# Kernel optimization log

Hardware: AMD Instinct MI355X
Metric: run time of the kernel (lower is better)

Reference implementation:

```python
import jax, jax.numpy as jnp
import numpy as np

K, N = 4096, 4096
GROUP_SIZE = 128
N_GROUPS = N // GROUP_SIZE  # 32
BATCH, SEQ = 4, 2048
NBITS = 4


def setup_inputs() -> dict:
    key = jax.random.key(0)
    ks = jax.random.split(key, 7)
    x = jax.random.normal(ks[0], (BATCH, SEQ, N), dtype=jnp.float32)
    W_q = jax.random.randint(ks[1], (K, N), 0, 2 ** NBITS, dtype=jnp.int32)
    scales = jax.random.uniform(ks[2], (K, N_GROUPS, 1), dtype=jnp.float32) * 0.05 + 0.001
    zeros = jax.random.uniform(ks[3], (K, N_GROUPS, 1), dtype=jnp.float32) * (2 ** NBITS)
    mu1 = jax.random.uniform(ks[4], (N,), dtype=jnp.float32) + 0.5  # per-column sinkhorn factor
    mu2 = jax.random.uniform(ks[5], (K,), dtype=jnp.float32) + 0.5  # per-row sinkhorn factor
    bias = jax.random.normal(ks[6], (K,), dtype=jnp.float32)
    return {"x": x, "W_q": W_q, "scales": scales, "zeros": zeros,
            "mu1": mu1, "mu2": mu2, "bias": bias}


def reference(x, W_q, scales, zeros, mu1, mu2, bias):
    input_dtype = x.dtype
    n_groups = scales.shape[1]
    group_size = W_q.shape[1] // n_groups
    # group-wise dequant: [K, n_groups, group_size]
    Q_g = W_q.astype(jnp.float32).reshape(K, n_groups, group_size)
    W_deq_norm = (Q_g - zeros) * scales
    # undo sinkhorn row/col normalization
    W_deq = W_deq_norm.reshape(K, N) * mu2[:, None] * mu1[None, :]
    W_deq = W_deq.astype(input_dtype)
    # linear: x [B,S,N] @ W_deq.T [N,K] + bias [K]
    return jnp.einsum('bsn,kn->bsk', x, W_deq) + bias
```

## Files before the change

kernel.cpp:

```cpp
#include <hip/hip_runtime.h>
#include <hip/hip_bf16.h>
#include <stdint.h>

#define M_DIM 8192
#define N_C   4096
#define K_OUT 4096
#define NGRP  32
#define NT    (N_C / 32)

typedef __attribute__((ext_vector_type(8))) short bf16x8;
typedef __attribute__((ext_vector_type(4))) float f32x4;

__device__ __forceinline__ unsigned short f2b(float f) {
  unsigned u = __float_as_uint(f);
  return (unsigned short)((u + 0x7fffu + ((u >> 16) & 1u)) >> 16);
}

__device__ __forceinline__ void gload_lds16(const void* g, void* l) {
  __builtin_amdgcn_global_load_lds(
      (const __attribute__((address_space(1))) void*)g,
      (__attribute__((address_space(3))) void*)l,
      16, 0, 0);
}

__global__ void convert_x_kernel(const float* __restrict__ x,
                                 unsigned short* __restrict__ xb) {
  const int total = (M_DIM * N_C) / 8;
  const int stride = gridDim.x * blockDim.x;
  for (int i = blockIdx.x * blockDim.x + threadIdx.x; i < total; i += stride) {
    const float4* p = (const float4*)(x + (size_t)i * 8);
    float4 a = p[0];
    float4 b = p[1];
    union { unsigned short u[8]; uint4 v; } o;
    o.u[0] = f2b(a.x); o.u[1] = f2b(a.y); o.u[2] = f2b(a.z); o.u[3] = f2b(a.w);
    o.u[4] = f2b(b.x); o.u[5] = f2b(b.y); o.u[6] = f2b(b.z); o.u[7] = f2b(b.w);
    *(uint4*)(xb + (size_t)i * 8) = o.v;
  }
}

__global__ void dequant_w_kernel(const int* __restrict__ Wq,
                                 const float* __restrict__ scales,
                                 const float* __restrict__ zeros,
                                 const float* __restrict__ mu1,
                                 const float* __restrict__ mu2,
                                 unsigned short* __restrict__ wb) {
  const int total = (K_OUT * N_C) / 8;
  const int stride = gridDim.x * blockDim.x;
  for (int i = blockIdx.x * blockDim.x + threadIdx.x; i < total; i += stride) {
    const int k  = i >> 9;
    const int nc = (i & 511) << 3;
    const int g  = nc >> 7;
    const float s = scales[k * NGRP + g];
    const float z = zeros[k * NGRP + g];
    const float f  = s * mu2[k];
    const float zf = z * f;
    const int4* q4 = (const int4*)(Wq + (size_t)k * N_C + nc);
    int4 q0 = q4[0], q1 = q4[1];
    const float4* m4 = (const float4*)(mu1 + nc);
    float4 m0 = m4[0], m1 = m4[1];
    union { unsigned short u[8]; uint4 v; } o;
    o.u[0] = f2b(((float)q0.x * f - zf) * m0.x);
    o.u[1] = f2b(((float)q0.y * f - zf) * m0.y);
    o.u[2] = f2b(((float)q0.z * f - zf) * m0.z);
    o.u[3] = f2b(((float)q0.w * f - zf) * m0.w);
    o.u[4] = f2b(((float)q1.x * f - zf) * m1.x);
    o.u[5] = f2b(((float)q1.y * f - zf) * m1.y);
    o.u[6] = f2b(((float)q1.z * f - zf) * m1.z);
    o.u[7] = f2b(((float)q1.w * f - zf) * m1.w);
    *(uint4*)(wb + (size_t)i * 8) = o.v;
  }
}

__global__ __launch_bounds__(512) void gemm_bf16_kernel(
    const unsigned short* __restrict__ Xb,
    const unsigned short* __restrict__ Wb,
    const float* __restrict__ bias,
    float* __restrict__ out) {
  __shared__ unsigned short smem[65536];

  const int bid = blockIdx.x;
  const int swz = (bid & 7) * 64 + (bid >> 3);
  const int n0 = (swz & 15) * 256;
  const int m0 = (swz >> 4) * 256;

  const int tid = threadIdx.x;
  const int w   = tid >> 6;
  const int l   = tid & 63;
  const int wr  = w >> 2;
  const int wc  = w & 3;

  const char* Xc = (const char*)Xb;
  const char* Wc = (const char*)Wb;
  const char* srcA[2];
  const char* srcB[2];
  int dstOff[2];
#pragma unroll
  for (int e = 0; e < 2; ++e) {
    const int P  = (e * 8 + w) * 1024 + l * 16;
    const int r  = P >> 6;
    const int sl = ((P >> 4) & 3) ^ ((r >> 1) & 3);
    srcA[e] = Xc + (size_t)(m0 + r) * (N_C * 2) + sl * 16;
    srcB[e] = Wc + (size_t)(n0 + r) * (N_C * 2) + sl * 16;
    dstOff[e] = (e * 8 + w) * 1024;
  }

  int offa[8], offb[4];
#pragma unroll
  for (int i = 0; i < 8; ++i) {
    const int r  = wr * 128 + i * 16 + (l & 15);
    const int sl = (l >> 4) ^ ((r >> 1) & 3);
    offa[i] = (r * 64 + sl * 16) >> 1;
  }
#pragma unroll
  for (int j = 0; j < 4; ++j) {
    const int r  = wc * 64 + j * 16 + (l & 15);
    const int sl = (l >> 4) ^ ((r >> 1) & 3);
    offb[j] = (16384 + r * 64 + sl * 16) >> 1;
  }

  f32x4 acc[8][4] = {};
  char* ldsc = (char*)smem;

#define STAGE(tt)                                                            \
  { const int sb = ((tt) & 3) * 32768; const size_t ko = (size_t)(tt) * 64;  \
    gload_lds16(srcA[0] + ko, ldsc + sb + dstOff[0]);                        \
    gload_lds16(srcA[1] + ko, ldsc + sb + dstOff[1]);                        \
    gload_lds16(srcB[0] + ko, ldsc + sb + 16384 + dstOff[0]);                \
    gload_lds16(srcB[1] + ko, ldsc + sb + 16384 + dstOff[1]); }

  STAGE(0)
  STAGE(1)
  STAGE(2)

#define KSTEP(VMSTR, tt, DOSTAGE)                                            \
  { asm volatile("s_waitcnt vmcnt(" VMSTR ")\n\ts_barrier" ::: "memory");    \
    const int bufo = ((tt) & 3) * 16384;                                     \
    bf16x8 af[8]; bf16x8 bfv[4];                                             \
    _Pragma("unroll") for (int i = 0; i < 8; ++i)                            \
      af[i] = *(const bf16x8*)(smem + bufo + offa[i]);                       \
    _Pragma("unroll") for (int j = 0; j < 4; ++j)                            \
      bfv[j] = *(const bf16x8*)(smem + bufo + offb[j]);                      \
    if (DOSTAGE) STAGE((tt) + 3)                                             \
    __builtin_amdgcn_s_setprio(1);                                           \
    _Pragma("unroll") for (int i = 0; i < 8; ++i)                            \
      _Pragma("unroll") for (int j = 0; j < 4; ++j)                          \
        acc[i][j] = __builtin_amdgcn_mfma_f32_16x16x32_bf16(af[i], bfv[j],   \
                                                            acc[i][j], 0, 0, 0); \
    __builtin_amdgcn_s_setprio(0); }

#pragma unroll 1
  for (int kt = 0; kt < NT - 3; ++kt) KSTEP("8", kt, 1)
  KSTEP("8", NT - 3, 0)
  KSTEP("4", NT - 2, 0)
  KSTEP("0", NT - 1, 0)

#undef KSTEP
#undef STAGE

#pragma unroll
  for (int j = 0; j < 4; ++j) {
    const int col = n0 + wc * 64 + j * 16 + (l & 15);
    const float bv = bias[col];
#pragma unroll
    for (int i = 0; i < 8; ++i) {
      const int row = m0 + wr * 128 + i * 16 + (l >> 4) * 4;
#pragma unroll
      for (int rr = 0; rr < 4; ++rr)
        out[(size_t)(row + rr) * K_OUT + col] = acc[i][j][rr] + bv;
    }
  }
}

extern "C" void kernel_launch(void* const* d_in, const int* in_sizes, int n_in,
                              void* d_out, int out_size, void* d_ws, size_t ws_size,
                              hipStream_t stream) {
  const float* x      = (const float*)d_in[0];
  const int*   Wq     = (const int*)d_in[1];
  const float* scales = (const float*)d_in[2];
  const float* zeros  = (const float*)d_in[3];
  const float* mu1    = (const float*)d_in[4];
  const float* mu2    = (const float*)d_in[5];
  const float* bias   = (const float*)d_in[6];
  float* out = (float*)d_out;

  unsigned short* xb = (unsigned short*)d_ws;
  unsigned short* wb = xb + (size_t)M_DIM * N_C;

  convert_x_kernel<<<2048, 256, 0, stream>>>(x, xb);
  dequant_w_kernel<<<2048, 256, 0, stream>>>(Wq, scales, zeros, mu1, mu2, wb);

  dim3 grid((M_DIM / 256) * (K_OUT / 256));
  gemm_bf16_kernel<<<grid, 512, 0, stream>>>(xb, wb, bias, out);
}
```

Baseline: 298.1 us.

## Restructure GEMM main loop into four-phase ping-pong schedule with 64-wide K tiles

Replaces the 4-deep K=32 ring-buffer pipeline with a double-buffered K=64 tile split into four phases (two M-halves by two K-halves). Each phase loads a slice of fragments, issues part of the next tile's global-to-LDS loads, and runs 16 MFMAs between barriers, so loads are spread across the compute. It also requests two workgroups per CU via launch bounds, which caps registers. The cost is more barriers per K step and possible register pressure or spills under the tighter bound; the accumulator row mapping is reordered to match.

```diff
diff --git a/kernel.cpp b/kernel.cpp
--- a/kernel.cpp
+++ b/kernel.cpp
@@ -6,7 +6,7 @@
 #define N_C   4096
 #define K_OUT 4096
 #define NGRP  32
-#define NT    (N_C / 32)
+#define NT64  (N_C / 64)
 
 typedef __attribute__((ext_vector_type(8))) short bf16x8;
 typedef __attribute__((ext_vector_type(4))) float f32x4;
@@ -71,7 +71,7 @@
   }
 }
 
-__global__ __launch_bounds__(512) void gemm_bf16_kernel(
+__global__ __launch_bounds__(512, 2) void gemm_bf16_kernel(
     const unsigned short* __restrict__ Xb,
     const unsigned short* __restrict__ Wb,
     const float* __restrict__ bias,
@@ -91,82 +91,101 @@
 
   const char* Xc = (const char*)Xb;
   const char* Wc = (const char*)Wb;
-  const char* srcA[2];
-  const char* srcB[2];
-  int dstOff[2];
-#pragma unroll
-  for (int e = 0; e < 2; ++e) {
-    const int P  = (e * 8 + w) * 1024 + l * 16;
-    const int r  = P >> 6;
-    const int sl = ((P >> 4) & 3) ^ ((r >> 1) & 3);
-    srcA[e] = Xc + (size_t)(m0 + r) * (N_C * 2) + sl * 16;
-    srcB[e] = Wc + (size_t)(n0 + r) * (N_C * 2) + sl * 16;
-    dstOff[e] = (e * 8 + w) * 1024;
-  }
-
-  int offa[8], offb[4];
-#pragma unroll
-  for (int i = 0; i < 8; ++i) {
-    const int r  = wr * 128 + i * 16 + (l & 15);
-    const int sl = (l >> 4) ^ ((r >> 1) & 3);
-    offa[i] = (r * 64 + sl * 16) >> 1;
-  }
-#pragma unroll
-  for (int j = 0; j < 4; ++j) {
-    const int r  = wc * 64 + j * 16 + (l & 15);
-    const int sl = (l >> 4) ^ ((r >> 1) & 3);
-    offb[j] = (16384 + r * 64 + sl * 16) >> 1;
-  }
+  char* ldsc = (char*)smem;
+
+  const int rowA0 = (w >> 2) * 128 + (w & 3) * 16 + (l >> 2);
+  const int rowB0 = w * 16 + (l >> 2);
+  const int slotA = (l & 3) ^ ((rowA0 >> 1) & 3);
+  const int slotB = (l & 3) ^ ((rowB0 >> 1) & 3);
+  const char* srcA0 = Xc + (size_t)(m0 + rowA0) * 8192 + slotA * 16;
+  const char* srcB0 = Wc + (size_t)(n0 + rowB0) * 8192 + slotB * 16;
+  const int dstA0 = rowA0 * 64 + (l & 3) * 16;
+  const int dstB0 = 32768 + rowB0 * 64 + (l & 3) * 16;
+
+  const int physk = (l >> 4) ^ (((l & 15) >> 1) & 3);
+  const int offA = (wr * 128 + (l & 15)) * 64 + physk * 16;
+  const int offB = 32768 + (wc * 64 + (l & 15)) * 64 + physk * 16;
 
   f32x4 acc[8][4] = {};
-  char* ldsc = (char*)smem;
-
-#define STAGE(tt)                                                            \
-  { const int sb = ((tt) & 3) * 32768; const size_t ko = (size_t)(tt) * 64;  \
-    gload_lds16(srcA[0] + ko, ldsc + sb + dstOff[0]);                        \
-    gload_lds16(srcA[1] + ko, ldsc + sb + dstOff[1]);                        \
-    gload_lds16(srcB[0] + ko, ldsc + sb + 16384 + dstOff[0]);                \
-    gload_lds16(srcB[1] + ko, ldsc + sb + 16384 + dstOff[1]); }
-
-  STAGE(0)
-  STAGE(1)
-  STAGE(2)
-
-#define KSTEP(VMSTR, tt, DOSTAGE)                                            \
-  { asm volatile("s_waitcnt vmcnt(" VMSTR ")\n\ts_barrier" ::: "memory");    \
-    const int bufo = ((tt) & 3) * 16384;                                     \
-    bf16x8 af[8]; bf16x8 bfv[4];                                             \
-    _Pragma("unroll") for (int i = 0; i < 8; ++i)                            \
-      af[i] = *(const bf16x8*)(smem + bufo + offa[i]);                       \
+  bf16x8 bfv[4];
+
+#define STG_P1(tt) { char* nb = ldsc + (((tt)+1)&1)*65536;                   \
+    const size_t ko = (size_t)((tt)+1)*128;                                  \
+    gload_lds16(srcA0 + ko, nb + dstA0);                                     \
+    gload_lds16(srcB0 + ko, nb + dstB0); }
+#define STG_P2(tt) { char* nb = ldsc + (((tt)+1)&1)*65536;                   \
+    const size_t ko = (size_t)((tt)+1)*128;                                  \
+    gload_lds16(srcB0 + 1048576 + ko, nb + dstB0 + 8192);                    \
+    gload_lds16(srcA0 + 524288 + ko, nb + dstA0 + 4096); }
+#define STG_P3(tt) { char* nb = ldsc + (((tt)+1)&1)*65536;                   \
+    const size_t ko = (size_t)((tt)+1)*128 + 64;                             \
+    gload_lds16(srcA0 + ko, nb + 16384 + dstA0);                             \
+    gload_lds16(srcB0 + ko, nb + 16384 + dstB0); }
+#define STG_P4(tt) { char* nb = ldsc + (((tt)+1)&1)*65536;                   \
+    const size_t ko = (size_t)((tt)+1)*128 + 64;                             \
+    gload_lds16(srcB0 + 1048576 + ko, nb + 16384 + dstB0 + 8192);            \
+    gload_lds16(srcA0 + 524288 + ko, nb + 16384 + dstA0 + 4096); }
+
+#define VM4 asm volatile("s_waitcnt vmcnt(4)" ::: "memory");
+#define VM0 asm volatile("s_waitcnt vmcnt(0)" ::: "memory");
+#define VMN ((void)0);
+
+#define PHASE(mh, kh, LOADB, tt, STG, VM)                                    \
+  { const int bufo = ((tt) & 1) * 65536;                                     \
+    if (LOADB) { _Pragma("unroll") for (int j = 0; j < 4; ++j)               \
+      bfv[j] = *(const bf16x8*)(ldsc + bufo + (kh)*16384 + offB + j*1024); } \
+    bf16x8 af[4];                                                            \
+    _Pragma("unroll") for (int i = 0; i < 4; ++i)                            \
+      af[i] = *(const bf16x8*)(ldsc + bufo + (kh)*16384 + offA + (mh)*4096 + i*1024); \
+    STG                                                                      \
+    VM                                                                       \
+    asm volatile("s_barrier" ::: "memory");                                  \
+    __builtin_amdgcn_s_setprio(1);                                           \
     _Pragma("unroll") for (int j = 0; j < 4; ++j)                            \
-      bfv[j] = *(const bf16x8*)(smem + bufo + offb[j]);                      \
-    if (DOSTAGE) STAGE((tt) + 3)                                             \
-    __builtin_amdgcn_s_setprio(1);                                           \
-    _Pragma("unroll") for (int i = 0; i < 8; ++i)                            \
-      _Pragma("unroll") for (int j = 0; j < 4; ++j)                          \
-        acc[i][j] = __builtin_amdgcn_mfma_f32_16x16x32_bf16(af[i], bfv[j],   \
-                                                            acc[i][j], 0, 0, 0); \
-    __builtin_amdgcn_s_setprio(0); }
+      _Pragma("unroll") for (int i = 0; i < 4; ++i)                          \
+        acc[(mh)*4+i][j] = __builtin_amdgcn_mfma_f32_16x16x32_bf16(          \
+            af[i], bfv[j], acc[(mh)*4+i][j], 0, 0, 0);                       \
+    __builtin_amdgcn_s_setprio(0);                                           \
+    asm volatile("s_barrier" ::: "memory"); }
+
+  gload_lds16(srcA0,                 ldsc + dstA0);
+  gload_lds16(srcB0,                 ldsc + dstB0);
+  gload_lds16(srcB0 + 1048576,       ldsc + dstB0 + 8192);
+  gload_lds16(srcA0 + 524288,        ldsc + dstA0 + 4096);
+  gload_lds16(srcA0 + 64,            ldsc + 16384 + dstA0);
+  gload_lds16(srcB0 + 64,            ldsc + 16384 + dstB0);
+  gload_lds16(srcB0 + 1048576 + 64,  ldsc + 16384 + dstB0 + 8192);
+  gload_lds16(srcA0 + 524288 + 64,   ldsc + 16384 + dstA0 + 4096);
+  asm volatile("s_waitcnt vmcnt(4)\n\ts_barrier" ::: "memory");
 
 #pragma unroll 1
-  for (int kt = 0; kt < NT - 3; ++kt) KSTEP("8", kt, 1)
-  KSTEP("8", NT - 3, 0)
-  KSTEP("4", NT - 2, 0)
-  KSTEP("0", NT - 1, 0)
-
-#undef KSTEP
-#undef STAGE
+  for (int kt = 0; kt < NT64 - 1; ++kt) {
+    PHASE(0, 0, 1, kt, STG_P1(kt), VMN)
+    PHASE(1, 0, 0, kt, STG_P2(kt), VM4)
+    PHASE(0, 1, 1, kt, STG_P3(kt), VMN)
+    PHASE(1, 1, 0, kt, STG_P4(kt), VM4)
+  }
+  PHASE(0, 0, 1, NT64 - 1, VMN, VMN)
+  PHASE(1, 0, 0, NT64 - 1, VMN, VM0)
+  PHASE(0, 1, 1, NT64 - 1, VMN, VMN)
+  PHASE(1, 1, 0, NT64 - 1, VMN, VMN)
+
+#undef PHASE
+#undef STG_P1
+#undef STG_P2
+#undef STG_P3
+#undef STG_P4
 
 #pragma unroll
   for (int j = 0; j < 4; ++j) {
     const int col = n0 + wc * 64 + j * 16 + (l & 15);
     const float bv = bias[col];
 #pragma unroll
-    for (int i = 0; i < 8; ++i) {
-      const int row = m0 + wr * 128 + i * 16 + (l >> 4) * 4;
+    for (int idx = 0; idx < 8; ++idx) {
+      const int row = m0 + wr * 128 + (idx >> 2) * 64 + (idx & 3) * 16 + (l >> 4) * 4;
 #pragma unroll
       for (int rr = 0; rr < 4; ++rr)
-        out[(size_t)(row + rr) * K_OUT + col] = acc[i][j][rr] + bv;
+        out[(size_t)(row + rr) * K_OUT + col] = acc[idx][j][rr] + bv;
     }
   }
 }
```

Result: slower. 306.0 us (+2.6%).

## Switch GEMM to 32x32x16 MFMA with K=16 stages and register double-buffering

Applied to the files above, without the earlier changes.

Replaces the 16x16x32 MFMA tiling with 32x32x16 bf16 MFMAs, which cuts LDS fragment loads per FLOP. The K step shrinks to 16, so each stage needs half the LDS (32KB total) and launch_bounds asks for two blocks per CU. LDS fragments are now prefetched into registers one iteration ahead, using ping-ponged register sets. The cost is twice as many barriers per K, smaller global loads per stage, and a possible register-pressure limit on the 2-block occupancy target.

```diff
diff --git a/kernel.cpp b/kernel.cpp
--- a/kernel.cpp
+++ b/kernel.cpp
@@ -6,10 +6,10 @@
 #define N_C   4096
 #define K_OUT 4096
 #define NGRP  32
-#define NT    (N_C / 32)
+#define NT16  (N_C / 16)
 
 typedef __attribute__((ext_vector_type(8))) short bf16x8;
-typedef __attribute__((ext_vector_type(4))) float f32x4;
+typedef __attribute__((ext_vector_type(16))) float f32x16;
 
 __device__ __forceinline__ unsigned short f2b(float f) {
   unsigned u = __float_as_uint(f);
@@ -71,12 +71,12 @@
   }
 }
 
-__global__ __launch_bounds__(512) void gemm_bf16_kernel(
+__global__ __launch_bounds__(512, 2) void gemm_bf16_kernel(
     const unsigned short* __restrict__ Xb,
     const unsigned short* __restrict__ Wb,
     const float* __restrict__ bias,
     float* __restrict__ out) {
-  __shared__ unsigned short smem[65536];
+  __shared__ unsigned short smem[32768];
 
   const int bid = blockIdx.x;
   const int swz = (bid & 7) * 64 + (bid >> 3);
@@ -91,82 +91,100 @@
 
   const char* Xc = (const char*)Xb;
   const char* Wc = (const char*)Wb;
-  const char* srcA[2];
-  const char* srcB[2];
-  int dstOff[2];
-#pragma unroll
-  for (int e = 0; e < 2; ++e) {
-    const int P  = (e * 8 + w) * 1024 + l * 16;
-    const int r  = P >> 6;
-    const int sl = ((P >> 4) & 3) ^ ((r >> 1) & 3);
-    srcA[e] = Xc + (size_t)(m0 + r) * (N_C * 2) + sl * 16;
-    srcB[e] = Wc + (size_t)(n0 + r) * (N_C * 2) + sl * 16;
-    dstOff[e] = (e * 8 + w) * 1024;
-  }
-
-  int offa[8], offb[4];
-#pragma unroll
-  for (int i = 0; i < 8; ++i) {
-    const int r  = wr * 128 + i * 16 + (l & 15);
-    const int sl = (l >> 4) ^ ((r >> 1) & 3);
-    offa[i] = (r * 64 + sl * 16) >> 1;
-  }
-#pragma unroll
-  for (int j = 0; j < 4; ++j) {
-    const int r  = wc * 64 + j * 16 + (l & 15);
-    const int sl = (l >> 4) ^ ((r >> 1) & 3);
-    offb[j] = (16384 + r * 64 + sl * 16) >> 1;
-  }
-
-  f32x4 acc[8][4] = {};
   char* ldsc = (char*)smem;
 
-#define STAGE(tt)                                                            \
-  { const int sb = ((tt) & 3) * 32768; const size_t ko = (size_t)(tt) * 64;  \
-    gload_lds16(srcA[0] + ko, ldsc + sb + dstOff[0]);                        \
-    gload_lds16(srcA[1] + ko, ldsc + sb + dstOff[1]);                        \
-    gload_lds16(srcB[0] + ko, ldsc + sb + 16384 + dstOff[0]);                \
-    gload_lds16(srcB[1] + ko, ldsc + sb + 16384 + dstOff[1]); }
+  const int rS   = w * 32 + (l >> 1);
+  const int sLog = (l & 1) ^ ((l >> 1) & 1);
+  const char* srcA0 = Xc + (size_t)(m0 + rS) * 8192 + sLog * 16;
+  const char* srcB0 = Wc + (size_t)(n0 + rS) * 8192 + sLog * 16;
+  const int dstA = w * 1024 + l * 16;
+  const int dstB = 8192 + dstA;
+
+  const int sbit = ((l >> 5) ^ (l & 1));
+  const int offA0 = (wr * 128 + (l & 31)) * 32 + sbit * 16;
+  const int offB0 = 8192 + (wc * 64 + (l & 31)) * 32 + sbit * 16;
+
+  f32x16 acc[4][2] = {};
+  bf16x8 S0a0, S0a1, S0a2, S0a3, S0b0, S0b1;
+  bf16x8 S1a0, S1a1, S1a2, S1a3, S1b0, S1b1;
+
+#define STAGE(tt) { char* nb = ldsc + ((tt) & 3) * 16384;                    \
+    const size_t ko = (size_t)(tt) * 32;                                     \
+    gload_lds16(srcA0 + ko, nb + dstA);                                      \
+    gload_lds16(srcB0 + ko, nb + dstB); }
+
+#define MFMA32(aa, bb, cc) __builtin_amdgcn_mfma_f32_32x32x16_bf16(aa, bb, cc, 0, 0, 0)
+
+#define ITER(VMSTR, tt, DOSTAGE, Ca0,Ca1,Ca2,Ca3,Cb0,Cb1, Na0,Na1,Na2,Na3,Nb0,Nb1) \
+  { asm volatile("s_waitcnt vmcnt(" VMSTR ")\n\ts_barrier" ::: "memory");    \
+    const char* bp = ldsc + (((tt) + 1) & 3) * 16384;                        \
+    Na0 = *(const bf16x8*)(bp + offA0);                                      \
+    Na1 = *(const bf16x8*)(bp + offA0 + 1024);                               \
+    Na2 = *(const bf16x8*)(bp + offA0 + 2048);                               \
+    Na3 = *(const bf16x8*)(bp + offA0 + 3072);                               \
+    Nb0 = *(const bf16x8*)(bp + offB0);                                      \
+    Nb1 = *(const bf16x8*)(bp + offB0 + 1024);                               \
+    if (DOSTAGE) STAGE((tt) + 3)                                             \
+    __builtin_amdgcn_s_setprio(1);                                           \
+    acc[0][0] = MFMA32(Ca0, Cb0, acc[0][0]);                                 \
+    acc[1][0] = MFMA32(Ca1, Cb0, acc[1][0]);                                 \
+    acc[2][0] = MFMA32(Ca2, Cb0, acc[2][0]);                                 \
+    acc[3][0] = MFMA32(Ca3, Cb0, acc[3][0]);                                 \
+    acc[0][1] = MFMA32(Ca0, Cb1, acc[0][1]);                                 \
+    acc[1][1] = MFMA32(Ca1, Cb1, acc[1][1]);                                 \
+    acc[2][1] = MFMA32(Ca2, Cb1, acc[2][1]);                                 \
+    acc[3][1] = MFMA32(Ca3, Cb1, acc[3][1]);                                 \
+    __builtin_amdgcn_s_setprio(0); }
 
   STAGE(0)
   STAGE(1)
   STAGE(2)
-
-#define KSTEP(VMSTR, tt, DOSTAGE)                                            \
-  { asm volatile("s_waitcnt vmcnt(" VMSTR ")\n\ts_barrier" ::: "memory");    \
-    const int bufo = ((tt) & 3) * 16384;                                     \
-    bf16x8 af[8]; bf16x8 bfv[4];                                             \
-    _Pragma("unroll") for (int i = 0; i < 8; ++i)                            \
-      af[i] = *(const bf16x8*)(smem + bufo + offa[i]);                       \
-    _Pragma("unroll") for (int j = 0; j < 4; ++j)                            \
-      bfv[j] = *(const bf16x8*)(smem + bufo + offb[j]);                      \
-    if (DOSTAGE) STAGE((tt) + 3)                                             \
-    __builtin_amdgcn_s_setprio(1);                                           \
-    _Pragma("unroll") for (int i = 0; i < 8; ++i)                            \
-      _Pragma("unroll") for (int j = 0; j < 4; ++j)                          \
-        acc[i][j] = __builtin_amdgcn_mfma_f32_16x16x32_bf16(af[i], bfv[j],   \
-                                                            acc[i][j], 0, 0, 0); \
-    __builtin_amdgcn_s_setprio(0); }
+  asm volatile("s_waitcnt vmcnt(4)\n\ts_barrier" ::: "memory");
+  {
+    const char* bp = ldsc;
+    S0a0 = *(const bf16x8*)(bp + offA0);
+    S0a1 = *(const bf16x8*)(bp + offA0 + 1024);
+    S0a2 = *(const bf16x8*)(bp + offA0 + 2048);
+    S0a3 = *(const bf16x8*)(bp + offA0 + 3072);
+    S0b0 = *(const bf16x8*)(bp + offB0);
+    S0b1 = *(const bf16x8*)(bp + offB0 + 1024);
+  }
 
 #pragma unroll 1
-  for (int kt = 0; kt < NT - 3; ++kt) KSTEP("8", kt, 1)
-  KSTEP("8", NT - 3, 0)
-  KSTEP("4", NT - 2, 0)
-  KSTEP("0", NT - 1, 0)
-
-#undef KSTEP
+  for (int t = 0; t < NT16 - 4; t += 2) {
+    ITER("2", t,     1, S0a0,S0a1,S0a2,S0a3,S0b0,S0b1, S1a0,S1a1,S1a2,S1a3,S1b0,S1b1)
+    ITER("2", t + 1, 1, S1a0,S1a1,S1a2,S1a3,S1b0,S1b1, S0a0,S0a1,S0a2,S0a3,S0b0,S0b1)
+  }
+  ITER("2", NT16 - 4, 1, S0a0,S0a1,S0a2,S0a3,S0b0,S0b1, S1a0,S1a1,S1a2,S1a3,S1b0,S1b1)
+  ITER("2", NT16 - 3, 0, S1a0,S1a1,S1a2,S1a3,S1b0,S1b1, S0a0,S0a1,S0a2,S0a3,S0b0,S0b1)
+  ITER("0", NT16 - 2, 0, S0a0,S0a1,S0a2,S0a3,S0b0,S0b1, S1a0,S1a1,S1a2,S1a3,S1b0,S1b1)
+  __builtin_amdgcn_s_setprio(1);
+  acc[0][0] = MFMA32(S1a0, S1b0, acc[0][0]);
+  acc[1][0] = MFMA32(S1a1, S1b0, acc[1][0]);
+  acc[2][0] = MFMA32(S1a2, S1b0, acc[2][0]);
+  acc[3][0] = MFMA32(S1a3, S1b0, acc[3][0]);
+  acc[0][1] = MFMA32(S1a0, S1b1, acc[0][1]);
+  acc[1][1] = MFMA32(S1a1, S1b1, acc[1][1]);
+  acc[2][1] = MFMA32(S1a2, S1b1, acc[2][1]);
+  acc[3][1] = MFMA32(S1a3, S1b1, acc[3][1]);
+  __builtin_amdgcn_s_setprio(0);
+
+#undef ITER
+#undef MFMA32
 #undef STAGE
 
 #pragma unroll
-  for (int j = 0; j < 4; ++j) {
-    const int col = n0 + wc * 64 + j * 16 + (l & 15);
+  for (int j = 0; j < 2; ++j) {
+    const int col = n0 + wc * 64 + j * 32 + (l & 31);
     const float bv = bias[col];
 #pragma unroll
-    for (int i = 0; i < 8; ++i) {
-      const int row = m0 + wr * 128 + i * 16 + (l >> 4) * 4;
+    for (int i = 0; i < 4; ++i) {
+      const int rbase = m0 + wr * 128 + i * 32 + 4 * (l >> 5);
 #pragma unroll
-      for (int rr = 0; rr < 4; ++rr)
-        out[(size_t)(row + rr) * K_OUT + col] = acc[i][j][rr] + bv;
+      for (int rr = 0; rr < 16; ++rr) {
+        const int row = rbase + (rr & 3) + 8 * (rr >> 2);
+        out[(size_t)row * K_OUT + col] = acc[i][j][rr] + bv;
+      }
     }
   }
 }
```

Result: slower. 375.7 us (+26.0%).

## Load GEMM B-tile straight to registers, halve LDS, target two blocks per CU

Applied to the files above, without the earlier changes.

Restructures the bf16 GEMM main loop so only the X (A) tile is staged through LDS with async global-to-LDS loads. The weight (B) fragments are now read from global memory directly into double-buffered registers. A fragments are prefetched one step ahead into a second register buffer. LDS use is halved and launch_bounds asks for two 512-thread blocks per CU to raise occupancy, and the block-to-tile mapping is changed. The cost is uncached per-lane strided global loads for B, duplicated across wave rows, plus a much tighter register budget that risks spills with a 128-float accumulator per thread.

```diff
diff --git a/kernel.cpp b/kernel.cpp
--- a/kernel.cpp
+++ b/kernel.cpp
@@ -71,17 +71,18 @@
   }
 }
 
-__global__ __launch_bounds__(512) void gemm_bf16_kernel(
+__global__ __launch_bounds__(512, 2) void gemm_bf16_kernel(
     const unsigned short* __restrict__ Xb,
     const unsigned short* __restrict__ Wb,
     const float* __restrict__ bias,
     float* __restrict__ out) {
-  __shared__ unsigned short smem[65536];
+  __shared__ unsigned short smem[32768];
 
   const int bid = blockIdx.x;
-  const int swz = (bid & 7) * 64 + (bid >> 3);
-  const int n0 = (swz & 15) * 256;
-  const int m0 = (swz >> 4) * 256;
+  const int x8  = bid & 7;
+  const int ii  = bid >> 3;
+  const int n0 = (2 * x8 + (ii >> 5)) * 256;
+  const int m0 = (ii & 31) * 256;
 
   const int tid = threadIdx.x;
   const int w   = tid >> 6;
@@ -91,71 +92,73 @@
 
   const char* Xc = (const char*)Xb;
   const char* Wc = (const char*)Wb;
+  char* ldsc = (char*)smem;
+
   const char* srcA[2];
-  const char* srcB[2];
   int dstOff[2];
 #pragma unroll
   for (int e = 0; e < 2; ++e) {
     const int P  = (e * 8 + w) * 1024 + l * 16;
     const int r  = P >> 6;
     const int sl = ((P >> 4) & 3) ^ ((r >> 1) & 3);
-    srcA[e] = Xc + (size_t)(m0 + r) * (N_C * 2) + sl * 16;
-    srcB[e] = Wc + (size_t)(n0 + r) * (N_C * 2) + sl * 16;
+    srcA[e] = Xc + (size_t)(m0 + r) * 8192 + sl * 16;
     dstOff[e] = (e * 8 + w) * 1024;
   }
 
-  int offa[8], offb[4];
-#pragma unroll
-  for (int i = 0; i < 8; ++i) {
-    const int r  = wr * 128 + i * 16 + (l & 15);
-    const int sl = (l >> 4) ^ ((r >> 1) & 3);
-    offa[i] = (r * 64 + sl * 16) >> 1;
-  }
-#pragma unroll
-  for (int j = 0; j < 4; ++j) {
-    const int r  = wc * 64 + j * 16 + (l & 15);
-    const int sl = (l >> 4) ^ ((r >> 1) & 3);
-    offb[j] = (16384 + r * 64 + sl * 16) >> 1;
-  }
+  const int r0   = wr * 128 + (l & 15);
+  const int sl0  = (l >> 4) ^ ((r0 >> 1) & 3);
+  const int offa0 = r0 * 64 + sl0 * 16;
+
+  const char* srcB = Wc + (size_t)(n0 + wc * 64 + (l & 15)) * 8192 + (l >> 4) * 16;
 
   f32x4 acc[8][4] = {};
-  char* ldsc = (char*)smem;
+  bf16x8 Ar[2][8];
+  bf16x8 Br[2][4];
 
-#define STAGE(tt)                                                            \
-  { const int sb = ((tt) & 3) * 32768; const size_t ko = (size_t)(tt) * 64;  \
-    gload_lds16(srcA[0] + ko, ldsc + sb + dstOff[0]);                        \
-    gload_lds16(srcA[1] + ko, ldsc + sb + dstOff[1]);                        \
-    gload_lds16(srcB[0] + ko, ldsc + sb + 16384 + dstOff[0]);                \
-    gload_lds16(srcB[1] + ko, ldsc + sb + 16384 + dstOff[1]); }
+#define STAGEA(tt) { char* nb = ldsc + ((tt) & 3) * 16384;                   \
+    const size_t ko = (size_t)(tt) * 64;                                     \
+    gload_lds16(srcA[0] + ko, nb + dstOff[0]);                               \
+    gload_lds16(srcA[1] + ko, nb + dstOff[1]); }
 
-  STAGE(0)
-  STAGE(1)
-  STAGE(2)
-
-#define KSTEP(VMSTR, tt, DOSTAGE)                                            \
+#define BODY(VMSTR, tt, CUR, NXT, DOREAD, DOLOADB, DOSTAGE)                  \
   { asm volatile("s_waitcnt vmcnt(" VMSTR ")\n\ts_barrier" ::: "memory");    \
-    const int bufo = ((tt) & 3) * 16384;                                     \
-    bf16x8 af[8]; bf16x8 bfv[4];                                             \
-    _Pragma("unroll") for (int i = 0; i < 8; ++i)                            \
-      af[i] = *(const bf16x8*)(smem + bufo + offa[i]);                       \
-    _Pragma("unroll") for (int j = 0; j < 4; ++j)                            \
-      bfv[j] = *(const bf16x8*)(smem + bufo + offb[j]);                      \
-    if (DOSTAGE) STAGE((tt) + 3)                                             \
+    if (DOREAD) { const char* bp = ldsc + (((tt) + 1) & 3) * 16384 + offa0;  \
+      _Pragma("unroll") for (int i = 0; i < 8; ++i)                          \
+        Ar[NXT][i] = *(const bf16x8*)(bp + i * 1024); }                      \
+    if (DOLOADB) { const char* q = srcB + (size_t)((tt) + 1) * 64;           \
+      _Pragma("unroll") for (int j = 0; j < 4; ++j)                          \
+        Br[NXT][j] = *(const bf16x8*)(q + (size_t)j * 131072); }             \
+    if (DOSTAGE) STAGEA((tt) + 3)                                            \
     __builtin_amdgcn_s_setprio(1);                                           \
     _Pragma("unroll") for (int i = 0; i < 8; ++i)                            \
       _Pragma("unroll") for (int j = 0; j < 4; ++j)                          \
-        acc[i][j] = __builtin_amdgcn_mfma_f32_16x16x32_bf16(af[i], bfv[j],   \
-                                                            acc[i][j], 0, 0, 0); \
+        acc[i][j] = __builtin_amdgcn_mfma_f32_16x16x32_bf16(Ar[CUR][i],      \
+            Br[CUR][j], acc[i][j], 0, 0, 0);                                 \
     __builtin_amdgcn_s_setprio(0); }
 
+  STAGEA(0)
+  STAGEA(1)
+  STAGEA(2)
+#pragma unroll
+  for (int j = 0; j < 4; ++j)
+    Br[0][j] = *(const bf16x8*)(srcB + (size_t)j * 131072);
+  asm volatile("s_waitcnt vmcnt(8)\n\ts_barrier" ::: "memory");
+#pragma unroll
+  for (int i = 0; i < 8; ++i)
+    Ar[0][i] = *(const bf16x8*)(ldsc + offa0 + i * 1024);
+
 #pragma unroll 1
-  for (int kt = 0; kt < NT - 3; ++kt) KSTEP("8", kt, 1)
-  KSTEP("8", NT - 3, 0)
-  KSTEP("4", NT - 2, 0)
-  KSTEP("0", NT - 1, 0)
+  for (int tp = 0; tp < NT / 2 - 2; ++tp) {
+    BODY("6", 2 * tp,     0, 1, 1, 1, 1)
+    BODY("6", 2 * tp + 1, 1, 0, 1, 1, 1)
+  }
+  BODY("6", NT - 4, 0, 1, 1, 1, 1)
+  BODY("6", NT - 3, 1, 0, 1, 1, 0)
+  BODY("4", NT - 2, 0, 1, 1, 1, 0)
+  BODY("0", NT - 1, 1, 0, 0, 0, 0)
 
-#undef KSTEP
-#undef STAGE
+#undef BODY
+#undef STAGEA
 
 #pragma unroll
   for (int j = 0; j < 4; ++j) {
```

After: 441.8 us. 48.2% more time.
